# Kernel optimization log

Hardware: AMD Instinct MI355X
Metric: run time of the kernel (lower is better)

Reference implementation:

```python
import jax, jax.numpy as jnp
import numpy as np

N_MB = 4  # number of micro-behavior buckets; C = N_MB**2 + 1

def setup_inputs() -> dict:
    key = jax.random.key(0)
    k_q, k_k, k_b, k_w, k_a = jax.random.split(key, 5)
    b, h, S, d = 8, 8, 512, 64
    C = N_MB * N_MB + 1
    return {
        "query": jax.random.normal(k_q, (b, h, S, d), dtype=jnp.float32),
        "key": jax.random.normal(k_k, (b, h, S, d), dtype=jnp.float32),
        "b_seq": jax.random.randint(k_b, (b, S), 0, N_MB + 1, dtype=jnp.int32),
        "W1": jax.random.normal(k_w, (N_MB, h, d, d), dtype=jnp.float32) * 0.02,
        "alpha1": jax.random.normal(k_a, (C, N_MB, h), dtype=jnp.float32) * 0.02,
    }

def reference(query, key, b_seq, W1, alpha1):
    # bucket-pair index per (i, j) token pair; 0 if either token is padding
    bi = b_seq[:, :, None]  # [b, S, 1]
    bj = b_seq[:, None, :]  # [b, 1, S]
    b_mat = ((bi - 1) * N_MB + bj) * (bi * bj != 0).astype(jnp.int32)  # [b, S, S]
    # mix the n_mb base bilinear weights into C per-bucket-pair matrices
    W1_ = jnp.einsum('Bhmn,CBh->Chmn', W1, jax.nn.softmax(alpha1, axis=1))
    # full bilinear score for every bucket-pair class C (the wasteful part)
    att_all = jnp.einsum('bhim,Chmn,bhjn->bhijC', query, W1_, key)  # [b,h,S,S,C]
    # select the score matching each pair's bucket index
    idx = b_mat[:, None, :, :, None].astype(jnp.int32)  # [b,1,S,S,1] -> broadcast over h
    idx = jnp.broadcast_to(idx, att_all.shape[:4] + (1,))
    scores = jnp.take_along_axis(att_all, idx, axis=4)[..., 0]  # [b,h,S,S]
    return scores
```

## Files before the change

### kernel.cpp

```cpp
#include <hip/hip_runtime.h>
#include <stdint.h>

#define NB 4
#define NC 17
#define HH 8
#define SS 512
#define DD 64
#define CT 64

typedef __attribute__((ext_vector_type(8))) short bf16x8;
typedef __attribute__((ext_vector_type(4))) float f32x4;

#define WS_W1   0
#define WS_RIDX 1114112
#define WS_GST  (WS_RIDX + 16384)

__device__ __forceinline__ unsigned short f2bf(float f) {
  unsigned int x; __builtin_memcpy(&x, &f, 4);
  return (unsigned short)((x + 0x7fff + ((x >> 16) & 1)) >> 16);
}
__device__ __forceinline__ bf16x8 cvt8(float4 a, float4 b) {
  union { bf16x8 v; unsigned short u[8]; } t;
  t.u[0] = f2bf(a.x); t.u[1] = f2bf(a.y); t.u[2] = f2bf(a.z); t.u[3] = f2bf(a.w);
  t.u[4] = f2bf(b.x); t.u[5] = f2bf(b.y); t.u[6] = f2bf(b.z); t.u[7] = f2bf(b.w);
  return t.v;
}

__global__ __launch_bounds__(256) void k_prep(const int* __restrict__ bseq,
                                              const float* __restrict__ W1,
                                              const float* __restrict__ alpha,
                                              int* __restrict__ ridx,
                                              int* __restrict__ gst,
                                              unsigned short* __restrict__ W1mbf) {
  int tid = threadIdx.x;
  if (blockIdx.x < 8) {
    int b = blockIdx.x;
    __shared__ int cnt[5], base[6], cur[5];
    if (tid < 5) cnt[tid] = 0;
    __syncthreads();
    for (int j = tid; j < SS; j += blockDim.x) atomicAdd(&cnt[bseq[b * SS + j]], 1);
    __syncthreads();
    if (tid == 0) {
      base[0] = 0;
      for (int k = 0; k < 5; k++) base[k + 1] = base[k] + cnt[k];
      for (int k = 0; k < 6; k++) gst[b * 6 + k] = base[k];
    }
    __syncthreads();
    if (tid < 5) cur[tid] = base[tid];
    __syncthreads();
    for (int j = tid; j < SS; j += blockDim.x) {
      int p = atomicAdd(&cur[bseq[b * SS + j]], 1);
      ridx[b * SS + p] = j;
    }
  } else {
    int cb = blockIdx.x - 8;
    int c = cb >> 3, hh = cb & 7;
    __shared__ float sm[NB];
    if (tid == 0) {
      float a[NB], mx = -1e30f;
      for (int B = 0; B < NB; B++) { a[B] = alpha[(c * NB + B) * HH + hh]; mx = fmaxf(mx, a[B]); }
      float s = 0.f;
      for (int B = 0; B < NB; B++) { a[B] = __expf(a[B] - mx); s += a[B]; }
      for (int B = 0; B < NB; B++) sm[B] = a[B] / s;
    }
    __syncthreads();
    float s0 = sm[0], s1 = sm[1], s2 = sm[2], s3 = sm[3];
    for (int idx = tid; idx < DD * DD; idx += blockDim.x) {
      float v = W1[((0 * HH + hh) * DD * DD) + idx] * s0 +
                W1[((1 * HH + hh) * DD * DD) + idx] * s1 +
                W1[((2 * HH + hh) * DD * DD) + idx] * s2 +
                W1[((3 * HH + hh) * DD * DD) + idx] * s3;
      W1mbf[((size_t)(c * HH + hh)) * DD * DD + idx] = f2bf(v);
    }
  }
}

__global__ __launch_bounds__(512, 4) void k_fused(const float* __restrict__ query,
                                                  const float* __restrict__ key,
                                                  const int* __restrict__ bseq,
                                                  const unsigned short* __restrict__ W1mbf,
                                                  const int* __restrict__ ridx,
                                                  const int* __restrict__ gst,
                                                  float* __restrict__ out) {
  int bx = blockIdx.x;
  int bh = bx & 63, jt = bx >> 6;
  int b = bh >> 3, h = bh & 7;
  int j0 = jt * CT;
  int tid = threadIdx.x, wave = tid >> 6, lane = tid & 63;
  int quad = lane >> 4, l16 = lane & 15;

  __shared__ __align__(16) unsigned short Tl[5][CT][72];
  __shared__ int ord[CT], lgs[6], cnt[5], cur[5];
  __shared__ int p1list[40], p2list[40];
  __shared__ int n1s[5], n1b[5], n1tot, n2tot;

  if (tid < 5) cnt[tid] = 0;
  __syncthreads();
  int mybj = 0;
  if (tid < CT) { mybj = bseq[b * SS + j0 + tid]; atomicAdd(&cnt[mybj], 1); }
  __syncthreads();
  if (tid == 0) {
    lgs[0] = 0;
    for (int a = 0; a < 5; a++) lgs[a + 1] = lgs[a] + cnt[a];
  }
  __syncthreads();
  if (tid < 5) cur[tid] = lgs[tid];
  __syncthreads();
  if (tid < CT) ord[atomicAdd(&cur[mybj], 1)] = tid;
  if (tid < 5) n1s[tid] = ((lgs[tid + 1] - lgs[tid] + 15) >> 4) * ((tid == 0) ? 1 : 5);
  __syncthreads();
  if (tid == 0) {
    int a0 = 0;
    for (int a = 0; a < 5; a++) { n1b[a] = a0; a0 += n1s[a]; }
    n1tot = a0;
    int a1 = 0;
    for (int a = 0; a < 5; a++) a1 += (gst[b * 6 + a + 1] - gst[b * 6 + a] + 15) >> 4;
    n2tot = a1;
  }
  __syncthreads();
  if (tid < 5) {
    int a = tid;
    int ls = lgs[a], le = lgs[a + 1];
    int w = n1b[a];
    for (int t0 = ls; t0 < le; t0 += 16) {
      if (a == 0) {
        p1list[w++] = t0 | (le << 6) | (1 << 21);
      } else {
        for (int B = 0; B < 5; B++) {
          int c = (B == 0) ? 0 : (B - 1) * NB + a;
          p1list[w++] = t0 | (le << 6) | (c << 13) | (B << 18);
        }
      }
    }
    int w2 = 0;
    for (int aa = 0; aa < a; aa++) w2 += (gst[b * 6 + aa + 1] - gst[b * 6 + aa] + 15) >> 4;
    int gs = gst[b * 6 + a], ge = gst[b * 6 + a + 1];
    for (int p0 = gs; p0 < ge; p0 += 16)
      p2list[w2++] = p0 | (ge << 10) | (a << 20);
  }
  __syncthreads();

  for (int idx = wave; idx < n1tot; idx += 8) {
    int e = p1list[idx];
    int t0 = e & 63, le = (e >> 6) & 127, c = (e >> 13) & 31, B = (e >> 18) & 7;
    int bc = (e >> 21) & 1;
    const unsigned short* Wc = W1mbf + ((size_t)(c * HH + h) << 12);
    int p = t0 + l16; if (p > le - 1) p = le - 1;
    int cl = ord[p];
    const float* kp = &key[((size_t)(bh * SS + j0 + cl)) * DD + quad * 8];
    float4 ka = *(const float4*)kp, kb = *(const float4*)(kp + 4);
    float4 kc = *(const float4*)(kp + 32), kd = *(const float4*)(kp + 36);
    bf16x8 af0 = cvt8(ka, kb);
    bf16x8 af1 = cvt8(kc, kd);
    int cr[4];
#pragma unroll
    for (int reg = 0; reg < 4; reg++) {
      int pr = t0 + quad * 4 + reg;
      cr[reg] = (pr < le) ? ord[pr] : -1;
    }
#pragma unroll
    for (int nt = 0; nt < 4; nt++) {
      const unsigned short* wp = &Wc[(nt * 16 + l16) * DD + quad * 8];
      bf16x8 b0 = *(const bf16x8*)wp;
      bf16x8 b1 = *(const bf16x8*)(wp + 32);
      f32x4 acc = {0.f, 0.f, 0.f, 0.f};
      acc = __builtin_amdgcn_mfma_f32_16x16x32_bf16(af0, b0, acc, 0, 0, 0);
      acc = __builtin_amdgcn_mfma_f32_16x16x32_bf16(af1, b1, acc, 0, 0, 0);
#pragma unroll
      for (int reg = 0; reg < 4; reg++) {
        if (cr[reg] >= 0) {
          unsigned short v = f2bf(acc[reg]);
          if (bc) {
#pragma unroll
            for (int Bw = 0; Bw < 5; Bw++) Tl[Bw][cr[reg]][nt * 16 + l16] = v;
          } else {
            Tl[B][cr[reg]][nt * 16 + l16] = v;
          }
        }
      }
    }
  }
  __syncthreads();

  for (int i0 = wave * 2; i0 < n2tot; i0 += 16) {
    int e0 = p2list[i0];
    bool has1 = (i0 + 1) < n2tot;
    int e1 = has1 ? p2list[i0 + 1] : e0;

    int p0a = e0 & 1023, gea = (e0 >> 10) & 1023, Ba = e0 >> 20;
    int p0b = e1 & 1023, geb = (e1 >> 10) & 1023, Bb = e1 >> 20;

    int pa = p0a + l16; if (pa > gea - 1) pa = gea - 1;
    int pb = p0b + l16; if (pb > geb - 1) pb = geb - 1;
    int ra = ridx[b * SS + pa];
    int rb = ridx[b * SS + pb];
    const float* qa = &query[((size_t)(bh * SS + ra)) * DD + quad * 8];
    const float* qb = &query[((size_t)(bh * SS + rb)) * DD + quad * 8];
    float4 a0 = *(const float4*)qa, a1 = *(const float4*)(qa + 4);
    float4 a2 = *(const float4*)(qa + 32), a3 = *(const float4*)(qa + 36);
    float4 b0_ = *(const float4*)qb, b1_ = *(const float4*)(qb + 4);
    float4 b2_ = *(const float4*)(qb + 32), b3_ = *(const float4*)(qb + 36);
    bf16x8 afa0 = cvt8(a0, a1), afa1 = cvt8(a2, a3);
    bf16x8 afb0 = cvt8(b0_, b1_), afb1 = cvt8(b2_, b3_);

    int rra[4], rrb[4];
#pragma unroll
    for (int reg = 0; reg < 4; reg++) {
      int pra = p0a + quad * 4 + reg;
      rra[reg] = (pra < gea) ? ridx[b * SS + pra] : -1;
      int prb = p0b + quad * 4 + reg;
      rrb[reg] = (has1 && prb < geb) ? ridx[b * SS + prb] : -1;
    }
#pragma unroll
    for (int ct = 0; ct < CT / 16; ct++) {
      const unsigned short* tpa = &Tl[Ba][ct * 16 + l16][quad * 8];
      const unsigned short* tpb = &Tl[Bb][ct * 16 + l16][quad * 8];
      bf16x8 ba0 = *(const bf16x8*)tpa;
      bf16x8 ba1 = *(const bf16x8*)(tpa + 32);
      bf16x8 bb0 = *(const bf16x8*)tpb;
      bf16x8 bb1 = *(const bf16x8*)(tpb + 32);
      f32x4 acca = {0.f, 0.f, 0.f, 0.f}, accb = {0.f, 0.f, 0.f, 0.f};
      acca = __builtin_amdgcn_mfma_f32_16x16x32_bf16(afa0, ba0, acca, 0, 0, 0);
      accb = __builtin_amdgcn_mfma_f32_16x16x32_bf16(afb0, bb0, accb, 0, 0, 0);
      acca = __builtin_amdgcn_mfma_f32_16x16x32_bf16(afa1, ba1, acca, 0, 0, 0);
      accb = __builtin_amdgcn_mfma_f32_16x16x32_bf16(afb1, bb1, accb, 0, 0, 0);
#pragma unroll
      for (int reg = 0; reg < 4; reg++) {
        if (rra[reg] >= 0)
          out[((size_t)(bh * SS + rra[reg])) * SS + j0 + ct * 16 + l16] = acca[reg];
        if (rrb[reg] >= 0)
          out[((size_t)(bh * SS + rrb[reg])) * SS + j0 + ct * 16 + l16] = accb[reg];
      }
    }
  }
}

extern "C" void kernel_launch(void* const* d_in, const int* in_sizes, int n_in,
                              void* d_out, int out_size, void* d_ws, size_t ws_size,
                              hipStream_t stream) {
  const float* q = (const float*)d_in[0];
  const float* k = (const float*)d_in[1];
  const int* bseq = (const int*)d_in[2];
  const float* W1 = (const float*)d_in[3];
  const float* alpha = (const float*)d_in[4];
  float* out = (float*)d_out;
  char* ws = (char*)d_ws;
  unsigned short* W1mbf = (unsigned short*)(ws + WS_W1);
  int* ridx = (int*)(ws + WS_RIDX);
  int* gst = (int*)(ws + WS_GST);

  hipLaunchKernelGGL(k_prep, dim3(8 + NC * HH), dim3(256), 0, stream,
                     bseq, W1, alpha, ridx, gst, W1mbf);
  hipLaunchKernelGGL(k_fused, dim3(64 * (SS / CT)), dim3(512), 0, stream,
                     q, k, bseq, W1mbf, ridx, gst, out);
}
```

Baseline: 119.8 us.

## Drop row sort; compute all five bucket products per row tile and select

Removes the global per-batch sort of query rows by bucket (ridx/gst) from the prep kernel. The fused kernel now walks query rows in natural order, computes the MFMA product against all five per-bucket T tiles, and picks the right one per row with selects. Block size drops from 512 to 256 threads and b_seq is staged in shared memory. The gathered query loads and scattered output writes become contiguous and coalesced, at the cost of about 2.5x more phase-2 MFMA work.

```diff
diff --git a/kernel.cpp b/kernel.cpp
--- a/kernel.cpp
+++ b/kernel.cpp
@@ -12,8 +12,6 @@
 typedef __attribute__((ext_vector_type(4))) float f32x4;
 
 #define WS_W1   0
-#define WS_RIDX 1114112
-#define WS_GST  (WS_RIDX + 16384)
 
 __device__ __forceinline__ unsigned short f2bf(float f) {
   unsigned int x; __builtin_memcpy(&x, &f, 4);
@@ -26,61 +24,35 @@
   return t.v;
 }
 
-__global__ __launch_bounds__(256) void k_prep(const int* __restrict__ bseq,
-                                              const float* __restrict__ W1,
+__global__ __launch_bounds__(256) void k_prep(const float* __restrict__ W1,
                                               const float* __restrict__ alpha,
-                                              int* __restrict__ ridx,
-                                              int* __restrict__ gst,
                                               unsigned short* __restrict__ W1mbf) {
   int tid = threadIdx.x;
-  if (blockIdx.x < 8) {
-    int b = blockIdx.x;
-    __shared__ int cnt[5], base[6], cur[5];
-    if (tid < 5) cnt[tid] = 0;
-    __syncthreads();
-    for (int j = tid; j < SS; j += blockDim.x) atomicAdd(&cnt[bseq[b * SS + j]], 1);
-    __syncthreads();
-    if (tid == 0) {
-      base[0] = 0;
-      for (int k = 0; k < 5; k++) base[k + 1] = base[k] + cnt[k];
-      for (int k = 0; k < 6; k++) gst[b * 6 + k] = base[k];
-    }
-    __syncthreads();
-    if (tid < 5) cur[tid] = base[tid];
-    __syncthreads();
-    for (int j = tid; j < SS; j += blockDim.x) {
-      int p = atomicAdd(&cur[bseq[b * SS + j]], 1);
-      ridx[b * SS + p] = j;
-    }
-  } else {
-    int cb = blockIdx.x - 8;
-    int c = cb >> 3, hh = cb & 7;
-    __shared__ float sm[NB];
-    if (tid == 0) {
-      float a[NB], mx = -1e30f;
-      for (int B = 0; B < NB; B++) { a[B] = alpha[(c * NB + B) * HH + hh]; mx = fmaxf(mx, a[B]); }
-      float s = 0.f;
-      for (int B = 0; B < NB; B++) { a[B] = __expf(a[B] - mx); s += a[B]; }
-      for (int B = 0; B < NB; B++) sm[B] = a[B] / s;
-    }
-    __syncthreads();
-    float s0 = sm[0], s1 = sm[1], s2 = sm[2], s3 = sm[3];
-    for (int idx = tid; idx < DD * DD; idx += blockDim.x) {
-      float v = W1[((0 * HH + hh) * DD * DD) + idx] * s0 +
-                W1[((1 * HH + hh) * DD * DD) + idx] * s1 +
-                W1[((2 * HH + hh) * DD * DD) + idx] * s2 +
-                W1[((3 * HH + hh) * DD * DD) + idx] * s3;
-      W1mbf[((size_t)(c * HH + hh)) * DD * DD + idx] = f2bf(v);
-    }
-  }
-}
-
-__global__ __launch_bounds__(512, 4) void k_fused(const float* __restrict__ query,
+  int cb = blockIdx.x;
+  int c = cb >> 3, hh = cb & 7;
+  __shared__ float sm[NB];
+  if (tid == 0) {
+    float a[NB], mx = -1e30f;
+    for (int B = 0; B < NB; B++) { a[B] = alpha[(c * NB + B) * HH + hh]; mx = fmaxf(mx, a[B]); }
+    float s = 0.f;
+    for (int B = 0; B < NB; B++) { a[B] = __expf(a[B] - mx); s += a[B]; }
+    for (int B = 0; B < NB; B++) sm[B] = a[B] / s;
+  }
+  __syncthreads();
+  float s0 = sm[0], s1 = sm[1], s2 = sm[2], s3 = sm[3];
+  for (int idx = tid; idx < DD * DD; idx += blockDim.x) {
+    float v = W1[((0 * HH + hh) * DD * DD) + idx] * s0 +
+              W1[((1 * HH + hh) * DD * DD) + idx] * s1 +
+              W1[((2 * HH + hh) * DD * DD) + idx] * s2 +
+              W1[((3 * HH + hh) * DD * DD) + idx] * s3;
+    W1mbf[((size_t)(c * HH + hh)) * DD * DD + idx] = f2bf(v);
+  }
+}
+
+__global__ __launch_bounds__(256, 4) void k_fused(const float* __restrict__ query,
                                                   const float* __restrict__ key,
                                                   const int* __restrict__ bseq,
                                                   const unsigned short* __restrict__ W1mbf,
-                                                  const int* __restrict__ ridx,
-                                                  const int* __restrict__ gst,
                                                   float* __restrict__ out) {
   int bx = blockIdx.x;
   int bh = bx & 63, jt = bx >> 6;
@@ -91,13 +63,15 @@
 
   __shared__ __align__(16) unsigned short Tl[5][CT][72];
   __shared__ int ord[CT], lgs[6], cnt[5], cur[5];
-  __shared__ int p1list[40], p2list[40];
-  __shared__ int n1s[5], n1b[5], n1tot, n2tot;
+  __shared__ int p1list[44], n1s[5], n1b[5], n1tot;
+  __shared__ int sb[SS];
+
+  for (int i = tid; i < SS; i += 256) sb[i] = bseq[b * SS + i];
 
   if (tid < 5) cnt[tid] = 0;
   __syncthreads();
   int mybj = 0;
-  if (tid < CT) { mybj = bseq[b * SS + j0 + tid]; atomicAdd(&cnt[mybj], 1); }
+  if (tid < CT) { mybj = sb[j0 + tid]; atomicAdd(&cnt[mybj], 1); }
   __syncthreads();
   if (tid == 0) {
     lgs[0] = 0;
@@ -113,9 +87,6 @@
     int a0 = 0;
     for (int a = 0; a < 5; a++) { n1b[a] = a0; a0 += n1s[a]; }
     n1tot = a0;
-    int a1 = 0;
-    for (int a = 0; a < 5; a++) a1 += (gst[b * 6 + a + 1] - gst[b * 6 + a] + 15) >> 4;
-    n2tot = a1;
   }
   __syncthreads();
   if (tid < 5) {
@@ -132,15 +103,10 @@
         }
       }
     }
-    int w2 = 0;
-    for (int aa = 0; aa < a; aa++) w2 += (gst[b * 6 + aa + 1] - gst[b * 6 + aa] + 15) >> 4;
-    int gs = gst[b * 6 + a], ge = gst[b * 6 + a + 1];
-    for (int p0 = gs; p0 < ge; p0 += 16)
-      p2list[w2++] = p0 | (ge << 10) | (a << 20);
-  }
-  __syncthreads();
-
-  for (int idx = wave; idx < n1tot; idx += 8) {
+  }
+  __syncthreads();
+
+  for (int idx = wave; idx < n1tot; idx += 4) {
     int e = p1list[idx];
     int t0 = e & 63, le = (e >> 6) & 127, c = (e >> 13) & 31, B = (e >> 18) & 7;
     int bc = (e >> 21) & 1;
@@ -182,54 +148,38 @@
   }
   __syncthreads();
 
-  for (int i0 = wave * 2; i0 < n2tot; i0 += 16) {
-    int e0 = p2list[i0];
-    bool has1 = (i0 + 1) < n2tot;
-    int e1 = has1 ? p2list[i0 + 1] : e0;
-
-    int p0a = e0 & 1023, gea = (e0 >> 10) & 1023, Ba = e0 >> 20;
-    int p0b = e1 & 1023, geb = (e1 >> 10) & 1023, Bb = e1 >> 20;
-
-    int pa = p0a + l16; if (pa > gea - 1) pa = gea - 1;
-    int pb = p0b + l16; if (pb > geb - 1) pb = geb - 1;
-    int ra = ridx[b * SS + pa];
-    int rb = ridx[b * SS + pb];
-    const float* qa = &query[((size_t)(bh * SS + ra)) * DD + quad * 8];
-    const float* qb = &query[((size_t)(bh * SS + rb)) * DD + quad * 8];
-    float4 a0 = *(const float4*)qa, a1 = *(const float4*)(qa + 4);
-    float4 a2 = *(const float4*)(qa + 32), a3 = *(const float4*)(qa + 36);
-    float4 b0_ = *(const float4*)qb, b1_ = *(const float4*)(qb + 4);
-    float4 b2_ = *(const float4*)(qb + 32), b3_ = *(const float4*)(qb + 36);
-    bf16x8 afa0 = cvt8(a0, a1), afa1 = cvt8(a2, a3);
-    bf16x8 afb0 = cvt8(b0_, b1_), afb1 = cvt8(b2_, b3_);
-
-    int rra[4], rrb[4];
-#pragma unroll
-    for (int reg = 0; reg < 4; reg++) {
-      int pra = p0a + quad * 4 + reg;
-      rra[reg] = (pra < gea) ? ridx[b * SS + pra] : -1;
-      int prb = p0b + quad * 4 + reg;
-      rrb[reg] = (has1 && prb < geb) ? ridx[b * SS + prb] : -1;
-    }
+  for (int rt = wave; rt < SS / 16; rt += 4) {
+    int p0 = rt * 16;
+    const float* qp = &query[((size_t)(bh * SS + p0 + l16)) * DD + quad * 8];
+    float4 a0 = *(const float4*)qp, a1 = *(const float4*)(qp + 4);
+    float4 a2 = *(const float4*)(qp + 32), a3 = *(const float4*)(qp + 36);
+    bf16x8 af0 = cvt8(a0, a1);
+    bf16x8 af1 = cvt8(a2, a3);
+    int Bq[4];
+#pragma unroll
+    for (int reg = 0; reg < 4; reg++) Bq[reg] = sb[p0 + quad * 4 + reg];
 #pragma unroll
     for (int ct = 0; ct < CT / 16; ct++) {
-      const unsigned short* tpa = &Tl[Ba][ct * 16 + l16][quad * 8];
-      const unsigned short* tpb = &Tl[Bb][ct * 16 + l16][quad * 8];
-      bf16x8 ba0 = *(const bf16x8*)tpa;
-      bf16x8 ba1 = *(const bf16x8*)(tpa + 32);
-      bf16x8 bb0 = *(const bf16x8*)tpb;
-      bf16x8 bb1 = *(const bf16x8*)(tpb + 32);
-      f32x4 acca = {0.f, 0.f, 0.f, 0.f}, accb = {0.f, 0.f, 0.f, 0.f};
-      acca = __builtin_amdgcn_mfma_f32_16x16x32_bf16(afa0, ba0, acca, 0, 0, 0);
-      accb = __builtin_amdgcn_mfma_f32_16x16x32_bf16(afb0, bb0, accb, 0, 0, 0);
-      acca = __builtin_amdgcn_mfma_f32_16x16x32_bf16(afa1, ba1, acca, 0, 0, 0);
-      accb = __builtin_amdgcn_mfma_f32_16x16x32_bf16(afb1, bb1, accb, 0, 0, 0);
+      f32x4 acc[5];
+#pragma unroll
+      for (int P = 0; P < 5; P++) {
+        const unsigned short* tp = &Tl[P][ct * 16 + l16][quad * 8];
+        bf16x8 tb0 = *(const bf16x8*)tp;
+        bf16x8 tb1 = *(const bf16x8*)(tp + 32);
+        f32x4 z = {0.f, 0.f, 0.f, 0.f};
+        z = __builtin_amdgcn_mfma_f32_16x16x32_bf16(af0, tb0, z, 0, 0, 0);
+        z = __builtin_amdgcn_mfma_f32_16x16x32_bf16(af1, tb1, z, 0, 0, 0);
+        acc[P] = z;
+      }
 #pragma unroll
       for (int reg = 0; reg < 4; reg++) {
-        if (rra[reg] >= 0)
-          out[((size_t)(bh * SS + rra[reg])) * SS + j0 + ct * 16 + l16] = acca[reg];
-        if (rrb[reg] >= 0)
-          out[((size_t)(bh * SS + rrb[reg])) * SS + j0 + ct * 16 + l16] = accb[reg];
+        int Bv = Bq[reg];
+        float v = acc[0][reg];
+        v = (Bv == 1) ? acc[1][reg] : v;
+        v = (Bv == 2) ? acc[2][reg] : v;
+        v = (Bv == 3) ? acc[3][reg] : v;
+        v = (Bv == 4) ? acc[4][reg] : v;
+        out[((size_t)(bh * SS + p0 + quad * 4 + reg)) * SS + j0 + ct * 16 + l16] = v;
       }
     }
   }
@@ -246,11 +196,8 @@
   float* out = (float*)d_out;
   char* ws = (char*)d_ws;
   unsigned short* W1mbf = (unsigned short*)(ws + WS_W1);
-  int* ridx = (int*)(ws + WS_RIDX);
-  int* gst = (int*)(ws + WS_GST);
-
-  hipLaunchKernelGGL(k_prep, dim3(8 + NC * HH), dim3(256), 0, stream,
-                     bseq, W1, alpha, ridx, gst, W1mbf);
-  hipLaunchKernelGGL(k_fused, dim3(64 * (SS / CT)), dim3(512), 0, stream,
-                     q, k, bseq, W1mbf, ridx, gst, out);
-}
+
+  hipLaunchKernelGGL(k_prep, dim3(NC * HH), dim3(256), 0, stream, W1, alpha, W1mbf);
+  hipLaunchKernelGGL(k_fused, dim3(64 * (SS / CT)), dim3(256), 0, stream,
+                     q, k, bseq, W1mbf, out);
+}
```

Measured after the change: 127.5 us. 6.4% more time.
